# Performance work log

Hardware: AMD Instinct MI355X
Metric: run time of the kernel (lower is better)

The kernel has to match this reference:

```python
import jax, jax.numpy as jnp
import numpy as np

N_NODES = 100000
N_EDGES = 800000
IN_DIM, HID_DIM, OUT_DIM = 256, 128, 64


def setup_inputs() -> dict:
    key = jax.random.key(0)
    k1, k2, k3, k4 = jax.random.split(key, 4)
    x = jax.random.normal(k1, (N_NODES, IN_DIM), dtype=jnp.float32)
    edge_index = jax.random.randint(k2, (2, N_EDGES), 0, N_NODES, dtype=jnp.int64)
    # Glorot-style init scaled params
    W1 = jax.random.normal(k3, (IN_DIM, HID_DIM), dtype=jnp.float32) * (1.0 / np.sqrt(IN_DIM))
    b1 = jnp.zeros((HID_DIM,), dtype=jnp.float32)
    W2 = jax.random.normal(k4, (HID_DIM, OUT_DIM), dtype=jnp.float32) * (1.0 / np.sqrt(HID_DIM))
    b2 = jnp.zeros((OUT_DIM,), dtype=jnp.float32)
    return {"x": x, "edge_index": edge_index, "W1": W1, "b1": b1, "W2": W2, "b2": b2}


def reference(x, edge_index, W1, b1, W2, b2):
    n = x.shape[0]
    # GCNConv default: add self-loops, symmetric normalization D^-1/2 (A+I) D^-1/2
    loop = jnp.arange(n, dtype=edge_index.dtype)
    src = jnp.concatenate([edge_index[0], loop])
    dst = jnp.concatenate([edge_index[1], loop])
    deg = jax.ops.segment_sum(jnp.ones(src.shape, dtype=x.dtype), dst, num_segments=n)
    dinv = jax.lax.rsqrt(deg)  # deg >= 1 thanks to self-loops
    norm = dinv[src] * dinv[dst]  # [E+N]

    def gcn_conv(h, W, b):
        hw = h @ W                                         # [N, d_out] dense transform first (d_out < d_in)
        msg = hw[src] * norm[:, None]                      # gather + scale, [E+N, d_out]
        agg = jax.ops.segment_sum(msg, dst, num_segments=n)
        return agg + b

    h = jax.nn.relu(gcn_conv(x, W1, b1))
    return gcn_conv(h, W2, b2)
```

## Files before the change

### kernel.cpp

```cpp
#include <hip/hip_runtime.h>

typedef unsigned int uint;
typedef unsigned short ushort;
typedef __attribute__((ext_vector_type(8))) short bf16x8;
typedef __attribute__((ext_vector_type(4))) float f32x4;

#define NN 100000
#define NE 800000
#define D_IN 256
#define D_HID 128
#define D_OUT 64

__device__ __forceinline__ ushort f2bf(float f) {
    uint u = __float_as_uint(f);
    return (ushort)((u + 0x7fffu + ((u >> 16) & 1u)) >> 16);
}
__device__ __forceinline__ float bflo(uint u) { return __uint_as_float(u << 16); }
__device__ __forceinline__ float bfhi(uint u) { return __uint_as_float(u & 0xffff0000u); }
__device__ __forceinline__ uint pack2(float lo, float hi) {
    return (uint)f2bf(lo) | ((uint)f2bf(hi) << 16);
}
__device__ __forceinline__ bf16x8 pack8(float4 a, float4 b) {
    bf16x8 r;
    r[0] = (short)f2bf(a.x); r[1] = (short)f2bf(a.y); r[2] = (short)f2bf(a.z); r[3] = (short)f2bf(a.w);
    r[4] = (short)f2bf(b.x); r[5] = (short)f2bf(b.y); r[6] = (short)f2bf(b.z); r[7] = (short)f2bf(b.w);
    return r;
}

__global__ __launch_bounds__(256) void k_count(const int* __restrict__ dst, int* __restrict__ count, int e) {
    int i = blockIdx.x * 256 + threadIdx.x;
    if (i < e) {
        unsigned d = (unsigned)dst[i];
        if (d < NN) atomicAdd(&count[d], 1);
    }
}

#define SCAN_B 1024
__global__ __launch_bounds__(SCAN_B) void k_scan1(const int* __restrict__ count, int* __restrict__ incl,
                                                  int* __restrict__ blocksum, int n) {
    __shared__ int tmp[SCAN_B];
    int t = threadIdx.x;
    int gid = blockIdx.x * SCAN_B + t;
    int v = (gid < n) ? count[gid] : 0;
    tmp[t] = v;
    __syncthreads();
    for (int off = 1; off < SCAN_B; off <<= 1) {
        int u = (t >= off) ? tmp[t - off] : 0;
        __syncthreads();
        tmp[t] += u;
        __syncthreads();
    }
    if (gid < n) incl[gid] = tmp[t];
    if (t == SCAN_B - 1) blocksum[blockIdx.x] = tmp[t];
}

__global__ __launch_bounds__(256) void k_scan3(const int* __restrict__ incl, const int* __restrict__ count,
                                               const int* __restrict__ blocksum, int nb, int* __restrict__ offsets,
                                               int* __restrict__ cursor, float* __restrict__ dinv, int n) {
    __shared__ int bs[128];
    int t = threadIdx.x;
    if (t < 128) bs[t] = (t < nb) ? blocksum[t] : 0;
    __syncthreads();
    int i = blockIdx.x * 256 + t;
    if (i < n) {
        int b = i >> 10;
        int off = 0;
        for (int j = 0; j < b; j++) off += bs[j];
        int inc = incl[i] + off;
        int exc = inc - count[i];
        offsets[i] = exc;
        cursor[i] = exc;
        dinv[i] = rsqrtf((float)(count[i] + 1));
        if (i == n - 1) offsets[n] = inc;
    }
}

__global__ __launch_bounds__(256) void k_scatter(const int* __restrict__ edges, int* __restrict__ cursor,
                                                 int* __restrict__ srcs, int e) {
    int i = blockIdx.x * 256 + threadIdx.x;
    if (i < e) {
        unsigned s = (unsigned)edges[i];
        unsigned d = (unsigned)edges[e + i];
        if (s < NN && d < NN) {
            int pos = atomicAdd(&cursor[d], 1);
            srcs[pos] = (int)s;
        }
    }
}

__global__ __launch_bounds__(256) void k_castW(const float* __restrict__ W1, const float* __restrict__ W2,
                                               ushort* __restrict__ w1t, ushort* __restrict__ w2t) {
    int t = blockIdx.x * 256 + threadIdx.x;
    if (t < D_IN * D_HID) {
        int n = t / D_IN, k = t % D_IN;
        w1t[t] = f2bf(W1[(size_t)k * D_HID + n]);
    } else {
        int u = t - D_IN * D_HID;
        if (u < D_HID * D_OUT) {
            int n = u / D_HID, k = u % D_HID;
            w2t[u] = f2bf(W2[(size_t)k * D_OUT + n]);
        }
    }
}

template <int K_DIM, int N_DIM, bool AF32, int MT>
__global__ __launch_bounds__(256) void k_gemm_stage(const void* __restrict__ Av, const ushort* __restrict__ BT,
                                                    const float* __restrict__ dinv, ushort* __restrict__ C, int M) {
    constexpr int NFW = N_DIM / 64;
    constexpr int KK = K_DIM / 32;
    constexpr int BR = MT * 16;
    constexpr int RB = K_DIM * (AF32 ? 4 : 2);
    constexpr int LDSB = BR * RB;
    constexpr int CH = LDSB / 16;
    __shared__ char lds[LDSB];

    const int tid = threadIdx.x;
    const int w = tid >> 6, lane = tid & 63;
    const int l15 = lane & 15, g = lane >> 4;
    const int row0 = blockIdx.x * BR;
    const int cb = w * 16 * NFW;

    bf16x8 bf[NFW][KK];
#pragma unroll
    for (int nf = 0; nf < NFW; nf++)
#pragma unroll
        for (int kk = 0; kk < KK; kk++)
            bf[nf][kk] = *reinterpret_cast<const bf16x8*>(
                BT + (size_t)(cb + nf * 16 + l15) * K_DIM + kk * 32 + g * 8);

    {
        const char* Ab = (const char*)Av;
#pragma unroll
        for (int i = 0; i < CH / 256; i++) {
            int c = (i * 4 + w) * 64 + lane;
            int p = c * 16;
            int r = p / RB;
            int off = p & (RB - 1);
            int f = (r & 7) << 4;
            int grow = min(row0 + r, M - 1);
            const char* src = Ab + (size_t)grow * RB + (off ^ f);
            __builtin_amdgcn_global_load_lds((const __attribute__((address_space(1))) void*)src,
                                             (__attribute__((address_space(3))) void*)(lds + p), 16, 0, 0);
        }
    }
    __syncthreads();

    f32x4 acc[MT][NFW];
#pragma unroll
    for (int mt = 0; mt < MT; mt++)
#pragma unroll
        for (int nf = 0; nf < NFW; nf++) acc[mt][nf] = (f32x4){0.f, 0.f, 0.f, 0.f};

#pragma unroll
    for (int kk = 0; kk < KK; kk++) {
#pragma unroll
        for (int mt = 0; mt < MT; mt++) {
            const int r = mt * 16 + l15;
            const int f = (r & 7) << 4;
            bf16x8 a;
            if constexpr (AF32) {
                const int o = kk * 128 + g * 32;
                float4 v0 = *(const float4*)(lds + r * RB + (o ^ f));
                float4 v1 = *(const float4*)(lds + r * RB + ((o + 16) ^ f));
                a = pack8(v0, v1);
            } else {
                const int o = kk * 64 + g * 16;
                a = *(const bf16x8*)(lds + r * RB + (o ^ f));
            }
#pragma unroll
            for (int nf = 0; nf < NFW; nf++)
                acc[mt][nf] = __builtin_amdgcn_mfma_f32_16x16x32_bf16(a, bf[nf][kk], acc[mt][nf], 0, 0, 0);
        }
    }

#pragma unroll
    for (int mt = 0; mt < MT; mt++) {
#pragma unroll
        for (int r4 = 0; r4 < 4; r4++) {
            int rr = row0 + mt * 16 + g * 4 + r4;
            if (rr < M) {
                float dv = dinv[rr];
#pragma unroll
                for (int nf = 0; nf < NFW; nf++)
                    C[(size_t)rr * N_DIM + cb + nf * 16 + l15] = f2bf(acc[mt][nf][r4] * dv);
            }
        }
    }
}

__global__ __launch_bounds__(256) void k_agg128(const ushort* __restrict__ hws, const int* __restrict__ srcs,
                                                const int* __restrict__ offs, const float* __restrict__ dinv,
                                                const float* __restrict__ bias, ushort* __restrict__ outb, int n) {
    const int wv = threadIdx.x >> 6, lane = threadIdx.x & 63;
    const int node = blockIdx.x * 4 + wv;
    if (node >= n) return;
    const int g = lane >> 4, l15 = lane & 15;
    const int beg = offs[node];
    const int T = offs[node + 1] - beg + 1;
    const uint4* base = (const uint4*)hws;
    float acc[8] = {};
    int t = g;
    for (; t + 4 < T; t += 8) {
        int s0 = (t == 0) ? node : srcs[beg + t - 1];
        int s1 = srcs[beg + t + 3];
        uint4 va = base[(size_t)s0 * 16 + l15];
        uint4 vb = base[(size_t)s1 * 16 + l15];
        acc[0] += bflo(va.x) + bflo(vb.x); acc[1] += bfhi(va.x) + bfhi(vb.x);
        acc[2] += bflo(va.y) + bflo(vb.y); acc[3] += bfhi(va.y) + bfhi(vb.y);
        acc[4] += bflo(va.z) + bflo(vb.z); acc[5] += bfhi(va.z) + bfhi(vb.z);
        acc[6] += bflo(va.w) + bflo(vb.w); acc[7] += bfhi(va.w) + bfhi(vb.w);
    }
    for (; t < T; t += 4) {
        int s0 = (t == 0) ? node : srcs[beg + t - 1];
        uint4 va = base[(size_t)s0 * 16 + l15];
        acc[0] += bflo(va.x); acc[1] += bfhi(va.x);
        acc[2] += bflo(va.y); acc[3] += bfhi(va.y);
        acc[4] += bflo(va.z); acc[5] += bfhi(va.z);
        acc[6] += bflo(va.w); acc[7] += bfhi(va.w);
    }
#pragma unroll
    for (int j = 0; j < 8; j++) {
        acc[j] += __shfl_xor(acc[j], 16);
        acc[j] += __shfl_xor(acc[j], 32);
    }
    if (g == 0) {
        const float dv = dinv[node];
        const float4* b4 = (const float4*)(bias + 8 * l15);
        float4 bb0 = b4[0], bb1 = b4[1];
        uint4 o;
        o.x = pack2(fmaxf(acc[0] * dv + bb0.x, 0.f), fmaxf(acc[1] * dv + bb0.y, 0.f));
        o.y = pack2(fmaxf(acc[2] * dv + bb0.z, 0.f), fmaxf(acc[3] * dv + bb0.w, 0.f));
        o.z = pack2(fmaxf(acc[4] * dv + bb1.x, 0.f), fmaxf(acc[5] * dv + bb1.y, 0.f));
        o.w = pack2(fmaxf(acc[6] * dv + bb1.z, 0.f), fmaxf(acc[7] * dv + bb1.w, 0.f));
        ((uint4*)outb)[(size_t)node * 16 + l15] = o;
    }
}

__global__ __launch_bounds__(256) void k_agg64(const ushort* __restrict__ hws, const int* __restrict__ srcs,
                                               const int* __restrict__ offs, const float* __restrict__ dinv,
                                               const float* __restrict__ bias, float* __restrict__ out, int n) {
    const int wv = threadIdx.x >> 6, lane = threadIdx.x & 63;
    const int node = blockIdx.x * 4 + wv;
    if (node >= n) return;
    const int g = lane >> 3, l7 = lane & 7;
    const int beg = offs[node];
    const int T = offs[node + 1] - beg + 1;
    const uint4* base = (const uint4*)hws;
    float acc[8] = {};
    int t = g;
    for (; t + 8 < T; t += 16) {
        int s0 = (t == 0) ? node : srcs[beg + t - 1];
        int s1 = srcs[beg + t + 7];
        uint4 va = base[(size_t)s0 * 8 + l7];
        uint4 vb = base[(size_t)s1 * 8 + l7];
        acc[0] += bflo(va.x) + bflo(vb.x); acc[1] += bfhi(va.x) + bfhi(vb.x);
        acc[2] += bflo(va.y) + bflo(vb.y); acc[3] += bfhi(va.y) + bfhi(vb.y);
        acc[4] += bflo(va.z) + bflo(vb.z); acc[5] += bfhi(va.z) + bfhi(vb.z);
        acc[6] += bflo(va.w) + bflo(vb.w); acc[7] += bfhi(va.w) + bfhi(vb.w);
    }
    for (; t < T; t += 8) {
        int s0 = (t == 0) ? node : srcs[beg + t - 1];
        uint4 va = base[(size_t)s0 * 8 + l7];
        acc[0] += bflo(va.x); acc[1] += bfhi(va.x);
        acc[2] += bflo(va.y); acc[3] += bfhi(va.y);
        acc[4] += bflo(va.z); acc[5] += bfhi(va.z);
        acc[6] += bflo(va.w); acc[7] += bfhi(va.w);
    }
#pragma unroll
    for (int j = 0; j < 8; j++) {
        acc[j] += __shfl_xor(acc[j], 8);
        acc[j] += __shfl_xor(acc[j], 16);
        acc[j] += __shfl_xor(acc[j], 32);
    }
    if (g == 0) {
        const float dv = dinv[node];
        const float4* b4 = (const float4*)(bias + 8 * l7);
        float4 bb0 = b4[0], bb1 = b4[1];
        float4 o0, o1;
        o0.x = acc[0] * dv + bb0.x; o0.y = acc[1] * dv + bb0.y;
        o0.z = acc[2] * dv + bb0.z; o0.w = acc[3] * dv + bb0.w;
        o1.x = acc[4] * dv + bb1.x; o1.y = acc[5] * dv + bb1.y;
        o1.z = acc[6] * dv + bb1.z; o1.w = acc[7] * dv + bb1.w;
        ((float4*)out)[(size_t)node * 16 + 2 * l7] = o0;
        ((float4*)out)[(size_t)node * 16 + 2 * l7 + 1] = o1;
    }
}

static inline size_t align_up(size_t x, size_t a) { return (x + a - 1) & ~(a - 1); }

extern "C" void kernel_launch(void* const* d_in, const int* in_sizes, int n_in,
                              void* d_out, int out_size, void* d_ws, size_t ws_size,
                              hipStream_t stream) {
    const float* x = (const float*)d_in[0];
    const int* edges = (const int*)d_in[1];
    const float* W1 = (const float*)d_in[2];
    const float* b1 = (const float*)d_in[3];
    const float* W2 = (const float*)d_in[4];
    const float* b2 = (const float*)d_in[5];
    float* out = (float*)d_out;

    char* p = (char*)d_ws;
    int* count = (int*)p;      p += align_up(NN * 4, 256);
    int* incl = (int*)p;       p += align_up(NN * 4, 256);
    int* offsets = (int*)p;    p += align_up((NN + 1) * 4, 256);
    int* cursor = (int*)p;     p += align_up(NN * 4, 256);
    int* srcs = (int*)p;       p += align_up(NE * 4, 256);
    int* blocksum = (int*)p;   p += align_up(256 * 4, 256);
    float* dinv = (float*)p;   p += align_up(NN * 4, 256);
    ushort* w1t = (ushort*)p;  p += align_up(D_IN * D_HID * 2, 256);
    ushort* w2t = (ushort*)p;  p += align_up(D_HID * D_OUT * 2, 256);
    ushort* hw1s = (ushort*)p; p += align_up((size_t)NN * D_HID * 2, 256);
    ushort* hb = (ushort*)p;   p += align_up((size_t)NN * D_HID * 2 + 32 * 1024, 256);
    ushort* hw2s = (ushort*)p; p += align_up((size_t)NN * D_OUT * 2, 256);

    const int nb_scan = (NN + SCAN_B - 1) / SCAN_B;

    hipMemsetAsync(count, 0, NN * 4, stream);
    k_count<<<(NE + 255) / 256, 256, 0, stream>>>(edges + NE, count, NE);
    k_scan1<<<nb_scan, SCAN_B, 0, stream>>>(count, incl, blocksum, NN);
    k_scan3<<<(NN + 255) / 256, 256, 0, stream>>>(incl, count, blocksum, nb_scan, offsets, cursor, dinv, NN);
    k_scatter<<<(NE + 255) / 256, 256, 0, stream>>>(edges, cursor, srcs, NE);
    k_castW<<<(D_IN * D_HID + D_HID * D_OUT + 255) / 256, 256, 0, stream>>>(W1, W2, w1t, w2t);

    k_gemm_stage<D_IN, D_HID, true, 4><<<(NN + 63) / 64, 256, 0, stream>>>(x, w1t, dinv, hw1s, NN);
    k_agg128<<<(NN + 3) / 4, 256, 0, stream>>>(hw1s, srcs, offsets, dinv, b1, hb, NN);

    k_gemm_stage<D_HID, D_OUT, false, 8><<<(NN + 127) / 128, 256, 0, stream>>>(hb, w2t, dinv, hw2s, NN);
    k_agg64<<<(NN + 3) / 4, 256, 0, stream>>>(hw2s, srcs, offsets, dinv, b2, out, NN);
}
```

Baseline: 381.5 us.

## Double-buffer GEMM A-tiles in LDS and give each wave one column slice

Replaces the single-shot GEMM kernel with a double-buffered version. Each block loads 16-row chunks of A into one of two LDS buffers, so the load of the next chunk overlaps MFMA work on the current one. Waves now own a single 16-column slice: 8 waves of 512 threads for layer 1, and a 64-row block instead of 128 for layer 2. This cuts register pressure and LDS footprint, which may raise occupancy. The cost is a barrier per chunk and each block reusing its B fragments over fewer rows.

New measurement: 371.5 us. 1.03x faster.

```diff
diff --git a/kernel.cpp b/kernel.cpp
--- a/kernel.cpp
+++ b/kernel.cpp
@@ -103,88 +103,81 @@
     }
 }
 
-template <int K_DIM, int N_DIM, bool AF32, int MT>
-__global__ __launch_bounds__(256) void k_gemm_stage(const void* __restrict__ Av, const ushort* __restrict__ BT,
-                                                    const float* __restrict__ dinv, ushort* __restrict__ C, int M) {
-    constexpr int NFW = N_DIM / 64;
+template <int K_DIM, int N_DIM, bool AF32, int WAVES, int NH>
+__global__ __launch_bounds__(WAVES * 64) void k_gemm_db(const void* __restrict__ Av, const ushort* __restrict__ BT,
+                                                        const float* __restrict__ dinv, ushort* __restrict__ C,
+                                                        int M) {
+    constexpr int THREADS = WAVES * 64;
     constexpr int KK = K_DIM / 32;
-    constexpr int BR = MT * 16;
     constexpr int RB = K_DIM * (AF32 ? 4 : 2);
-    constexpr int LDSB = BR * RB;
-    constexpr int CH = LDSB / 16;
-    __shared__ char lds[LDSB];
+    constexpr int HB = 16 * RB;
+    constexpr int CPT = HB / 16 / THREADS;
+    constexpr int BR = NH * 16;
+    __shared__ char lds[2 * HB];
 
     const int tid = threadIdx.x;
     const int w = tid >> 6, lane = tid & 63;
     const int l15 = lane & 15, g = lane >> 4;
     const int row0 = blockIdx.x * BR;
-    const int cb = w * 16 * NFW;
-
-    bf16x8 bf[NFW][KK];
-#pragma unroll
-    for (int nf = 0; nf < NFW; nf++)
-#pragma unroll
-        for (int kk = 0; kk < KK; kk++)
-            bf[nf][kk] = *reinterpret_cast<const bf16x8*>(
-                BT + (size_t)(cb + nf * 16 + l15) * K_DIM + kk * 32 + g * 8);
-
-    {
-        const char* Ab = (const char*)Av;
-#pragma unroll
-        for (int i = 0; i < CH / 256; i++) {
-            int c = (i * 4 + w) * 64 + lane;
+    const int colw = w * 16;
+
+    bf16x8 bf[KK];
+#pragma unroll
+    for (int kk = 0; kk < KK; kk++)
+        bf[kk] = *reinterpret_cast<const bf16x8*>(BT + (size_t)(colw + l15) * K_DIM + kk * 32 + g * 8);
+
+    const char* Ab = (const char*)Av;
+    const int fme = (l15 & 7) << 4;
+
+    auto stage = [&](char* buf, int h) {
+#pragma unroll
+        for (int i = 0; i < CPT; i++) {
+            int c = i * THREADS + tid;
             int p = c * 16;
             int r = p / RB;
-            int off = p & (RB - 1);
+            int off = p - r * RB;
             int f = (r & 7) << 4;
-            int grow = min(row0 + r, M - 1);
+            int grow = min(row0 + h * 16 + r, M - 1);
             const char* src = Ab + (size_t)grow * RB + (off ^ f);
             __builtin_amdgcn_global_load_lds((const __attribute__((address_space(1))) void*)src,
-                                             (__attribute__((address_space(3))) void*)(lds + p), 16, 0, 0);
-        }
-    }
-    __syncthreads();
-
-    f32x4 acc[MT][NFW];
-#pragma unroll
-    for (int mt = 0; mt < MT; mt++)
-#pragma unroll
-        for (int nf = 0; nf < NFW; nf++) acc[mt][nf] = (f32x4){0.f, 0.f, 0.f, 0.f};
-
-#pragma unroll
-    for (int kk = 0; kk < KK; kk++) {
-#pragma unroll
-        for (int mt = 0; mt < MT; mt++) {
-            const int r = mt * 16 + l15;
-            const int f = (r & 7) << 4;
+                                             (__attribute__((address_space(3))) void*)(buf + p), 16, 0, 0);
+        }
+    };
+
+    auto compute = [&](const char* buf, int h) {
+        f32x4 acc = (f32x4){0.f, 0.f, 0.f, 0.f};
+#pragma unroll
+        for (int kk = 0; kk < KK; kk++) {
             bf16x8 a;
             if constexpr (AF32) {
                 const int o = kk * 128 + g * 32;
-                float4 v0 = *(const float4*)(lds + r * RB + (o ^ f));
-                float4 v1 = *(const float4*)(lds + r * RB + ((o + 16) ^ f));
+                float4 v0 = *(const float4*)(buf + l15 * RB + (o ^ fme));
+                float4 v1 = *(const float4*)(buf + l15 * RB + ((o + 16) ^ fme));
                 a = pack8(v0, v1);
             } else {
                 const int o = kk * 64 + g * 16;
-                a = *(const bf16x8*)(lds + r * RB + (o ^ f));
+                a = *(const bf16x8*)(buf + l15 * RB + (o ^ fme));
             }
-#pragma unroll
-            for (int nf = 0; nf < NFW; nf++)
-                acc[mt][nf] = __builtin_amdgcn_mfma_f32_16x16x32_bf16(a, bf[nf][kk], acc[mt][nf], 0, 0, 0);
-        }
-    }
-
-#pragma unroll
-    for (int mt = 0; mt < MT; mt++) {
+            acc = __builtin_amdgcn_mfma_f32_16x16x32_bf16(a, bf[kk], acc, 0, 0, 0);
+        }
 #pragma unroll
         for (int r4 = 0; r4 < 4; r4++) {
-            int rr = row0 + mt * 16 + g * 4 + r4;
-            if (rr < M) {
-                float dv = dinv[rr];
-#pragma unroll
-                for (int nf = 0; nf < NFW; nf++)
-                    C[(size_t)rr * N_DIM + cb + nf * 16 + l15] = f2bf(acc[mt][nf][r4] * dv);
-            }
-        }
+            int rr = row0 + h * 16 + g * 4 + r4;
+            if (rr < M) C[(size_t)rr * N_DIM + colw + l15] = f2bf(acc[r4] * dinv[rr]);
+        }
+    };
+
+    char* b0 = lds;
+    char* b1 = lds + HB;
+    stage(b0, 0);
+    __syncthreads();
+#pragma unroll
+    for (int h = 0; h < NH; h++) {
+        const char* cur = (h & 1) ? b1 : b0;
+        char* nxt = (h & 1) ? b0 : b1;
+        if (h + 1 < NH) stage(nxt, h + 1);
+        compute(cur, h);
+        __syncthreads();
     }
 }
 
@@ -322,9 +315,11 @@
     k_scatter<<<(NE + 255) / 256, 256, 0, stream>>>(edges, cursor, srcs, NE);
     k_castW<<<(D_IN * D_HID + D_HID * D_OUT + 255) / 256, 256, 0, stream>>>(W1, W2, w1t, w2t);
 
-    k_gemm_stage<D_IN, D_HID, true, 4><<<(NN + 63) / 64, 256, 0, stream>>>(x, w1t, dinv, hw1s, NN);
+    const int gemm_blocks = (NN + 63) / 64;
+
+    k_gemm_db<D_IN, D_HID, true, 8, 4><<<gemm_blocks, 512, 0, stream>>>(x, w1t, dinv, hw1s, NN);
     k_agg128<<<(NN + 3) / 4, 256, 0, stream>>>(hw1s, srcs, offsets, dinv, b1, hb, NN);
 
-    k_gemm_stage<D_HID, D_OUT, false, 8><<<(NN + 127) / 128, 256, 0, stream>>>(hb, w2t, dinv, hw2s, NN);
+    k_gemm_db<D_HID, D_OUT, false, 4, 4><<<gemm_blocks, 256, 0, stream>>>(hb, w2t, dinv, hw2s, NN);
     k_agg64<<<(NN + 3) / 4, 256, 0, stream>>>(hw2s, srcs, offsets, dinv, b2, out, NN);
 }
```
